# Kernel optimization log

Measured on AMD Instinct MI355X. Metric: run time of the kernel, lower is better.

## Reference

```python
import jax, jax.numpy as jnp
import numpy as np

N = 100000
E = 1600000
IN_DIM, HID, OUT = 128, 64, 32
SLOPE = 0.1


def setup_inputs() -> dict:
    key = jax.random.key(0)
    ks = jax.random.split(key, 8)
    x = jax.random.normal(ks[0], (N, IN_DIM), dtype=jnp.float32)
    edge_index = jax.random.randint(ks[1], (2, E), 0, N, dtype=jnp.int64)
    s1 = 1.0 / np.sqrt(IN_DIM)
    s2 = 1.0 / np.sqrt(HID)
    W_l1 = jax.random.uniform(ks[2], (IN_DIM, HID), jnp.float32, -s1, s1)
    W_r1 = jax.random.uniform(ks[3], (IN_DIM, HID), jnp.float32, -s1, s1)
    b1 = jax.random.uniform(ks[4], (HID,), jnp.float32, -s1, s1)
    W_l2 = jax.random.uniform(ks[5], (HID, OUT), jnp.float32, -s2, s2)
    W_r2 = jax.random.uniform(ks[6], (HID, OUT), jnp.float32, -s2, s2)
    b2 = jax.random.uniform(ks[7], (OUT,), jnp.float32, -s2, s2)
    return {"x": x, "edge_index": edge_index,
            "W_l1": W_l1, "W_r1": W_r1, "b1": b1,
            "W_l2": W_l2, "W_r2": W_r2, "b2": b2}


def _sage_conv(h, src, dst, deg_inv, W_l, W_r, b):
    # mean-aggregate neighbor features: gather from src, scatter-add to dst
    agg = jax.ops.segment_sum(h[src], dst, num_segments=N) * deg_inv  # [N, d]
    return agg @ W_l + h @ W_r + b


def reference(x, edge_index, W_l1, W_r1, b1, W_l2, W_r2, b2):
    src, dst = edge_index[0], edge_index[1]
    deg = jax.ops.segment_sum(jnp.ones((E,), x.dtype), dst, num_segments=N)
    deg_inv = (1.0 / jnp.maximum(deg, 1.0))[:, None]  # [N, 1]
    h = jax.nn.leaky_relu(_sage_conv(x, src, dst, deg_inv, W_l1, W_r1, b1), SLOPE)
    z = jax.nn.leaky_relu(_sage_conv(h, src, dst, deg_inv, W_l2, W_r2, b2), SLOPE)
    return z
```

## Files before the change

### kernel.cpp

```cpp
#include <hip/hip_runtime.h>


constexpr int IN_DIM  = 128;
constexpr int HID     = 64;
constexpr int OUT_DIM = 32;
constexpr float SLOPE = 0.1f;
constexpr int NPB_SHIFT = 8;
constexpr int NBMAX = 512;
constexpr int CHUNK = 4096;
constexpr int SUBCAP = 4096;

typedef unsigned int uint32;
typedef unsigned short ushort16;
typedef unsigned char uchar8;
using floatx2 = __attribute__((ext_vector_type(2))) float;

__device__ inline float blo(uint32 u) { return __uint_as_float(u << 16); }
__device__ inline float bhi(uint32 u) { return __uint_as_float(u & 0xffff0000u); }
__device__ inline ushort16 f2b(float f) {
    uint32 u = __float_as_uint(f);
    u += 0x7fffu + ((u >> 16) & 1u);
    return (ushort16)(u >> 16);
}
__device__ inline uint32 pack2(float lo, float hi) {
    return (uint32)f2b(lo) | ((uint32)f2b(hi) << 16);
}
__device__ inline float lrelu(float v) { return (v > 0.f) ? v : SLOPE * v; }
__device__ inline void addup(float* acc, uint4 u) {
    acc[0] += blo(u.x); acc[1] += bhi(u.x);
    acc[2] += blo(u.y); acc[3] += bhi(u.y);
    acc[4] += blo(u.z); acc[5] += bhi(u.z);
    acc[6] += blo(u.w); acc[7] += bhi(u.w);
}
__device__ inline uchar8 f2fp8(float f) {
    uint32 r = (uint32)__builtin_amdgcn_cvt_pk_fp8_f32(f, f, 0, false);
    return (uchar8)(r & 0xffu);
}
__device__ inline void addp4(float* acc, uint32 w) {
    floatx2 a = __builtin_amdgcn_cvt_pk_f32_fp8((int)w, false);
    floatx2 b = __builtin_amdgcn_cvt_pk_f32_fp8((int)w, true);
    acc[0] += a[0]; acc[1] += a[1]; acc[2] += b[0]; acc[3] += b[1];
}
__device__ inline void addq8(float* acc, uint2 u) {
    addp4(acc + 0, u.x); addp4(acc + 4, u.y);
}

__global__ __launch_bounds__(256) void prep_kernel(
    const float* __restrict__ Wl1, const float* __restrict__ Wr1,
    const float* __restrict__ Wl2, const float* __restrict__ Wr2,
    ushort16* __restrict__ Wb1, ushort16* __restrict__ Wb2,
    int* __restrict__ bhist, int* __restrict__ done) {
    const int gid = blockIdx.x * 256 + threadIdx.x;
    if (gid < NBMAX) bhist[gid] = 0;
    if (gid == NBMAX) *done = 0;
    for (int i = gid; i < 128 * 128; i += gridDim.x * 256) {
        int c = i >> 7, k = i & 127;
        Wb1[i] = f2b((c < HID) ? Wl1[k * HID + c] : Wr1[k * HID + (c - HID)]);
    }
    for (int i = gid; i < 64 * 64; i += gridDim.x * 256) {
        int c = i >> 6, k = i & 63;
        Wb2[i] = f2b((c < OUT_DIM) ? Wl2[k * OUT_DIM + c]
                                   : Wr2[k * OUT_DIM + (c - OUT_DIM)]);
    }
}

__global__ __launch_bounds__(256) void hist_scan_kernel(
    const int* __restrict__ dst, int* __restrict__ bhist,
    int* __restrict__ pbase, int* __restrict__ bcur,
    int* __restrict__ done, int E, int NB) {
    __shared__ int bh[NBMAX];
    __shared__ int s2[256];
    __shared__ int flag;
    const int tid = threadIdx.x;
    for (int i = tid; i < NBMAX; i += 256) bh[i] = 0;
    __syncthreads();
    for (int e = blockIdx.x * 256 + tid; e < E; e += gridDim.x * 256)
        atomicAdd(&bh[dst[e] >> NPB_SHIFT], 1);
    __syncthreads();
    for (int b = tid; b < NBMAX; b += 256)
        if (bh[b]) atomicAdd(&bhist[b], bh[b]);
    __threadfence();
    if (tid == 0) flag = (atomicAdd(done, 1) == (int)gridDim.x - 1) ? 1 : 0;
    __syncthreads();
    if (!flag) return;
    __threadfence();
    int v0 = atomicAdd(&bhist[2 * tid], 0);
    int v1 = atomicAdd(&bhist[2 * tid + 1], 0);
    int p0 = (v0 + 15) & ~15, p1 = (v1 + 15) & ~15;
    s2[tid] = p0 + p1; __syncthreads();
    for (int off = 1; off < 256; off <<= 1) {
        int b = (tid >= off) ? s2[tid - off] : 0;
        __syncthreads();
        s2[tid] += b;
        __syncthreads();
    }
    int base = s2[tid] - (p0 + p1);
    pbase[2 * tid]     = base;      bcur[2 * tid]     = base;
    pbase[2 * tid + 1] = base + p0; bcur[2 * tid + 1] = base + p0;
}

__global__ __launch_bounds__(256) void gemm1_part_kernel(
    const float* __restrict__ x, const ushort16* __restrict__ Wb1,
    const float* __restrict__ b1,
    const int* __restrict__ src, const int* __restrict__ dst,
    int* __restrict__ bcur, uint32* __restrict__ pairs,
    ushort16* __restrict__ xl, ushort16* __restrict__ xr,
    int N, int E, int NB, int npart) {
    using frag = __attribute__((ext_vector_type(8))) short;
    using f32x4 = __attribute__((ext_vector_type(4))) float;
    constexpr int LDA = IN_DIM + 8;
    __shared__ union {
        struct {
            int hist[NBMAX], loff[NBMAX], cur[NBMAX], gbase[NBMAX];
            int s[256];
            uint32 stage[CHUNK];
        } p;
        ushort16 Ash[64][LDA];
        ushort16 xst[2][64][64];
    } sm;
    const int tid = threadIdx.x;
    if (blockIdx.x < npart) {
        const int e0  = blockIdx.x * CHUNK;
        const int cnt = min(CHUNK, E - e0);
        for (int i = tid; i < NBMAX; i += 256) sm.p.hist[i] = 0;
        __syncthreads();
        int sreg[16], dreg[16];
#pragma unroll
        for (int k = 0; k < 16; ++k) {
            int i = tid + k * 256;
            if (i < cnt) {
                sreg[k] = src[e0 + i];
                dreg[k] = dst[e0 + i];
                atomicAdd(&sm.p.hist[dreg[k] >> NPB_SHIFT], 1);
            }
        }
        __syncthreads();
        int a0 = sm.p.hist[2 * tid], a1 = sm.p.hist[2 * tid + 1];
        sm.p.s[tid] = a0 + a1; __syncthreads();
        for (int off = 1; off < 256; off <<= 1) {
            int t = (tid >= off) ? sm.p.s[tid - off] : 0;
            __syncthreads();
            sm.p.s[tid] += t;
            __syncthreads();
        }
        int ex = sm.p.s[tid] - (a0 + a1);
        sm.p.loff[2 * tid] = ex;      sm.p.loff[2 * tid + 1] = ex + a0;
        sm.p.cur[2 * tid]  = ex;      sm.p.cur[2 * tid + 1]  = ex + a0;
        __syncthreads();
#pragma unroll
        for (int k = 0; k < 16; ++k) {
            int i = tid + k * 256;
            if (i < cnt) {
                int b = dreg[k] >> NPB_SHIFT;
                int pos = atomicAdd(&sm.p.cur[b], 1);
                sm.p.stage[pos] = (uint32)sreg[k] | ((uint32)(dreg[k] & 255) << 24);
            }
        }
        __syncthreads();
        for (int b = tid; b < NB; b += 256) {
            int cb = sm.p.hist[b];
            if (cb) sm.p.gbase[b] = atomicAdd(&bcur[b], cb);
        }
        __syncthreads();
        for (int i = tid; i < cnt; i += 256) {
            int lo = 0, hi = NB - 1;
            while (lo < hi) {
                int mid = (lo + hi + 1) >> 1;
                if (sm.p.loff[mid] <= i) lo = mid; else hi = mid - 1;
            }
            pairs[sm.p.gbase[lo] + (i - sm.p.loff[lo])] = sm.p.stage[i];
        }
        return;
    }
    const int n0 = (blockIdx.x - npart) * 64;
    {
        const int lc = (tid & 31) * 4;
        for (int row = tid >> 5; row < 64; row += 8) {
            int node = n0 + row;
            float4 xv = (node < N)
                ? *reinterpret_cast<const float4*>(&x[(long)node * IN_DIM + lc])
                : float4{0.f, 0.f, 0.f, 0.f};
            ushort16 pk[4] = {f2b(xv.x), f2b(xv.y), f2b(xv.z), f2b(xv.w)};
            *reinterpret_cast<ushort2*>(&sm.Ash[row][lc])     = ushort2{pk[0], pk[1]};
            *reinterpret_cast<ushort2*>(&sm.Ash[row][lc + 2]) = ushort2{pk[2], pk[3]};
        }
    }
    __syncthreads();
    const int lane = tid & 63;
    const int m0   = (tid >> 6) * 16;
    const int mlo  = lane & 15;
    const int qk   = lane >> 4;
    frag Af[4];
#pragma unroll
    for (int kc = 0; kc < 4; ++kc)
        Af[kc] = *reinterpret_cast<const frag*>(&sm.Ash[m0 + mlo][kc * 32 + qk * 8]);
    __syncthreads();
#pragma unroll
    for (int ct = 0; ct < 8; ++ct) {
        f32x4 acc = {0.f, 0.f, 0.f, 0.f};
#pragma unroll
        for (int kc = 0; kc < 4; ++kc) {
            frag Bf = *reinterpret_cast<const frag*>(
                &Wb1[(ct * 16 + mlo) * 128 + kc * 32 + qk * 8]);
            acc = __builtin_amdgcn_mfma_f32_16x16x32_bf16(Af[kc], Bf, acc, 0, 0, 0);
        }
        const int col = ct * 16 + mlo;
#pragma unroll
        for (int r = 0; r < 4; ++r) {
            int row = m0 + qk * 4 + r;
            if (col < HID) sm.xst[0][row][col] = f2b(acc[r]);
            else           sm.xst[1][row][col - HID] = f2b(acc[r] + b1[col - HID]);
        }
    }
    __syncthreads();
    for (int idx = tid; idx < 64 * 8; idx += 256) {
        int row = idx >> 3, ch = idx & 7;
        int node = n0 + row;
        if (node < N) {
            reinterpret_cast<uint4*>(xl)[(long)node * 8 + ch] =
                reinterpret_cast<const uint4*>(&sm.xst[0][0][0])[idx];
            reinterpret_cast<uint4*>(xr)[(long)node * 8 + ch] =
                reinterpret_cast<const uint4*>(&sm.xst[1][0][0])[idx];
        }
    }
}

__global__ __launch_bounds__(512) void agg1_gemm2_kernel(
    const uint32* __restrict__ pairs, const int* __restrict__ bhist,
    const int* __restrict__ pbase,
    const uint4* __restrict__ xlq, const uint4* __restrict__ xrq,
    const ushort16* __restrict__ Wb2, const float* __restrict__ b2,
    uint32* __restrict__ srcs, int* __restrict__ rowptr, int* __restrict__ degA,
    uchar8* __restrict__ hl8, ushort16* __restrict__ hr, int N) {
    using frag = __attribute__((ext_vector_type(8))) short;
    using f32x4 = __attribute__((ext_vector_type(4))) float;
    constexpr int LDH = HID + 8;
    __shared__ int hist[256], loff[256], cur[128];
    __shared__ int lsrc[SUBCAP];
    __shared__ ushort16 hsh[128][LDH];
    const int tid  = threadIdx.x;
    const int bkt  = blockIdx.x >> 1;
    const int half = blockIdx.x & 1;
    const int n0   = bkt << NPB_SHIFT;
    const int base = pbase[bkt];
    const int sz   = bhist[bkt];
    if (tid < 256) hist[tid] = 0;
    __syncthreads();
    for (int i = tid; i < sz; i += 512)
        atomicAdd(&hist[pairs[base + i] >> 24], 1);
    __syncthreads();
    int v = (tid < 256) ? hist[tid] : 0;
    if (tid < 256) loff[tid] = v;
    __syncthreads();
    for (int off = 1; off < 256; off <<= 1) {
        int t = (tid >= off && tid < 256) ? loff[tid - off] : 0;
        __syncthreads();
        if (tid < 256) loff[tid] += t;
        __syncthreads();
    }
    if (tid < 256) loff[tid] -= v;
    __syncthreads();
    if (half == 0 && tid < 256 && n0 + tid < N) {
        rowptr[n0 + tid] = base + loff[tid];
        degA[n0 + tid]   = hist[tid];
    }
    const int hbase = loff[half << 7];
    const int hcnt  = (half ? sz : loff[128]) - hbase;
    if (tid < 128) cur[tid] = loff[(half << 7) + tid] - hbase;
    __syncthreads();
    for (int i = tid; i < sz; i += 512) {
        uint32 u = pairs[base + i];
        int dl = u >> 24;
        if ((dl >> 7) == half) {
            int pos = atomicAdd(&cur[dl & 127], 1);
            lsrc[pos] = (int)(u & 0xFFFFFFu);
        }
    }
    __syncthreads();
    for (int i = tid; i < hcnt; i += 512)
        srcs[base + hbase + i] = (uint32)lsrc[i];
    const int lane = tid & 63;
    const int wid  = tid >> 6;
    const int li   = lane & 7;
#pragma unroll
    for (int pass = 0; pass < 2; ++pass) {
        const int nll = pass * 64 + wid * 8 + (lane >> 3);
        const int nl  = (half << 7) + nll;
        const int n   = n0 + nl;
        if (n >= N) continue;
        const int lo0 = loff[nl] - hbase;
        const int d   = hist[nl];
        float acc[8] = {};
        int j = 0;
        while (j + 16 <= d) {
            int i0[8], i1[8];
#pragma unroll
            for (int t = 0; t < 8; ++t) i0[t] = lsrc[lo0 + j + t];
#pragma unroll
            for (int t = 0; t < 8; ++t) i1[t] = lsrc[lo0 + j + 8 + t];
            uint4 u0[8], u1[8];
#pragma unroll
            for (int t = 0; t < 8; ++t) u0[t] = xlq[(long)i0[t] * 8 + li];
#pragma unroll
            for (int t = 0; t < 8; ++t) u1[t] = xlq[(long)i1[t] * 8 + li];
#pragma unroll
            for (int t = 0; t < 8; ++t) { addup(acc, u0[t]); addup(acc, u1[t]); }
            j += 16;
        }
        if (j + 8 <= d) {
            int i0[8];
#pragma unroll
            for (int t = 0; t < 8; ++t) i0[t] = lsrc[lo0 + j + t];
            uint4 u0[8];
#pragma unroll
            for (int t = 0; t < 8; ++t) u0[t] = xlq[(long)i0[t] * 8 + li];
#pragma unroll
            for (int t = 0; t < 8; ++t) addup(acc, u0[t]);
            j += 8;
        }
        for (; j < d; ++j) {
            uint4 u = xlq[(long)lsrc[lo0 + j] * 8 + li];
            addup(acc, u);
        }
        const float dinv = (d > 0) ? (1.f / (float)d) : 1.f;
        uint4 xv = xrq[(long)n * 8 + li];
        float h[8];
        h[0] = fmaf(acc[0], dinv, blo(xv.x)); h[1] = fmaf(acc[1], dinv, bhi(xv.x));
        h[2] = fmaf(acc[2], dinv, blo(xv.y)); h[3] = fmaf(acc[3], dinv, bhi(xv.y));
        h[4] = fmaf(acc[4], dinv, blo(xv.z)); h[5] = fmaf(acc[5], dinv, bhi(xv.z));
        h[6] = fmaf(acc[6], dinv, blo(xv.w)); h[7] = fmaf(acc[7], dinv, bhi(xv.w));
#pragma unroll
        for (int t = 0; t < 8; ++t) h[t] = lrelu(h[t]);
        uint4 pk;
        pk.x = pack2(h[0], h[1]); pk.y = pack2(h[2], h[3]);
        pk.z = pack2(h[4], h[5]); pk.w = pack2(h[6], h[7]);
        *reinterpret_cast<uint4*>(&hsh[nll][li * 8]) = pk;
    }
    __syncthreads();
    unsigned char* hl_st = reinterpret_cast<unsigned char*>(lsrc);
    ushort16* hr_st = reinterpret_cast<ushort16*>(lsrc + 1024);
    const int m0  = wid * 16;
    const int mlo = lane & 15;
    const int qk  = lane >> 4;
    frag Af[2];
#pragma unroll
    for (int kc = 0; kc < 2; ++kc)
        Af[kc] = *reinterpret_cast<const frag*>(&hsh[m0 + mlo][kc * 32 + qk * 8]);
#pragma unroll
    for (int ct = 0; ct < 4; ++ct) {
        f32x4 acc = {0.f, 0.f, 0.f, 0.f};
#pragma unroll
        for (int kc = 0; kc < 2; ++kc) {
            frag Bf = *reinterpret_cast<const frag*>(
                &Wb2[(ct * 16 + mlo) * 64 + kc * 32 + qk * 8]);
            acc = __builtin_amdgcn_mfma_f32_16x16x32_bf16(Af[kc], Bf, acc, 0, 0, 0);
        }
        const int col = ct * 16 + mlo;
#pragma unroll
        for (int r = 0; r < 4; ++r) {
            int row = m0 + qk * 4 + r;
            if (col < OUT_DIM) hl_st[row * 32 + col] = f2fp8(acc[r]);
            else hr_st[row * 32 + (col - OUT_DIM)] = f2b(acc[r] + b2[col - OUT_DIM]);
        }
    }
    __syncthreads();
    for (int idx = tid; idx < 128 * 2; idx += 512) {
        int row = idx >> 1, ch = idx & 1;
        int node = n0 + (half << 7) + row;
        if (node < N)
            reinterpret_cast<uint4*>(hl8)[(long)node * 2 + ch] =
                reinterpret_cast<const uint4*>(hl_st)[idx];
    }
    for (int idx = tid; idx < 128 * 4; idx += 512) {
        int row = idx >> 2, ch = idx & 3;
        int node = n0 + (half << 7) + row;
        if (node < N)
            reinterpret_cast<uint4*>(hr)[(long)node * 4 + ch] =
                reinterpret_cast<const uint4*>(hr_st)[idx];
    }
}

__global__ __launch_bounds__(256) void agg2_final_kernel(
    const int* __restrict__ rowptr, const int* __restrict__ degA,
    const uint32* __restrict__ srcs,
    const uint2* __restrict__ hlq, const uint4* __restrict__ hrq,
    float* __restrict__ z, int N) {
    const int lane  = threadIdx.x & 63;
    const int li    = lane & 3;
    const int gbase = lane & 60;
    const int wave  = (blockIdx.x << 2) + (threadIdx.x >> 6);
    const int n     = wave * 16 + (lane >> 2);
    if (n >= N) return;
    const int rp = rowptr[n];
    const int d  = degA[n];
    float acc[8] = {};
    int j = 0;
    while (j + 16 <= d) {
        int sA = (int)srcs[rp + j + li];
        int sB = (int)srcs[rp + j + 4 + li];
        int sC = (int)srcs[rp + j + 8 + li];
        int sD = (int)srcs[rp + j + 12 + li];
        uint2 u[16];
#pragma unroll
        for (int t = 0; t < 4; ++t) u[t]      = hlq[(long)__shfl(sA, gbase + t) * 4 + li];
#pragma unroll
        for (int t = 0; t < 4; ++t) u[4 + t]  = hlq[(long)__shfl(sB, gbase + t) * 4 + li];
#pragma unroll
        for (int t = 0; t < 4; ++t) u[8 + t]  = hlq[(long)__shfl(sC, gbase + t) * 4 + li];
#pragma unroll
        for (int t = 0; t < 4; ++t) u[12 + t] = hlq[(long)__shfl(sD, gbase + t) * 4 + li];
#pragma unroll
        for (int t = 0; t < 16; ++t) addq8(acc, u[t]);
        j += 16;
    }
    while (j + 4 <= d) {
        int sA = (int)srcs[rp + j + li];
        uint2 u[4];
#pragma unroll
        for (int t = 0; t < 4; ++t) u[t] = hlq[(long)__shfl(sA, gbase + t) * 4 + li];
#pragma unroll
        for (int t = 0; t < 4; ++t) addq8(acc, u[t]);
        j += 4;
    }
    int r = d - j;
    if (r > 0) {
        int sA = (int)srcs[rp + j + ((li < r) ? li : 0)];
#pragma unroll
        for (int t = 0; t < 3; ++t) {
            if (t < r) {
                uint2 u = hlq[(long)__shfl(sA, gbase + t) * 4 + li];
                addq8(acc, u);
            }
        }
    }
    const float dinv = (d > 0) ? (1.f / (float)d) : 1.f;
    uint4 hv = hrq[(long)n * 4 + li];
    float4 vA, vB;
    vA.x = lrelu(fmaf(acc[0], dinv, blo(hv.x))); vA.y = lrelu(fmaf(acc[1], dinv, bhi(hv.x)));
    vA.z = lrelu(fmaf(acc[2], dinv, blo(hv.y))); vA.w = lrelu(fmaf(acc[3], dinv, bhi(hv.y)));
    vB.x = lrelu(fmaf(acc[4], dinv, blo(hv.z))); vB.y = lrelu(fmaf(acc[5], dinv, bhi(hv.z)));
    vB.z = lrelu(fmaf(acc[6], dinv, blo(hv.w))); vB.w = lrelu(fmaf(acc[7], dinv, bhi(hv.w)));
    *reinterpret_cast<float4*>(&z[(long)n * OUT_DIM + 8 * li]) = vA;
    *reinterpret_cast<float4*>(&z[(long)n * OUT_DIM + 8 * li + 4]) = vB;
}

extern "C" void kernel_launch(void* const* d_in, const int* in_sizes, int n_in,
                              void* d_out, int out_size, void* d_ws, size_t ws_size,
                              hipStream_t stream) {
    const float* x   = (const float*)d_in[0];
    const int*   ei  = (const int*)d_in[1];
    const float* Wl1 = (const float*)d_in[2];
    const float* Wr1 = (const float*)d_in[3];
    const float* b1  = (const float*)d_in[4];
    const float* Wl2 = (const float*)d_in[5];
    const float* Wr2 = (const float*)d_in[6];
    const float* b2  = (const float*)d_in[7];

    const int N = in_sizes[0] / IN_DIM;
    const int E = in_sizes[1] / 2;
    const int* src = ei;
    const int* dst = ei + E;
    const int NB = (N + 255) >> NPB_SHIFT;

    char* p = (char*)d_ws;
    int* bhist    = (int*)p;           p += sizeof(int) * NBMAX;
    int* done     = (int*)p;           p += sizeof(int) * 4;
    int* pbase    = (int*)p;           p += sizeof(int) * NBMAX;
    int* bcur     = (int*)p;           p += sizeof(int) * NBMAX;
    int* rowptr   = (int*)p;           p += sizeof(int) * (N + 4);
    int* degA     = (int*)p;           p += sizeof(int) * (N + 4);
    uint32* pairs = (uint32*)p;        p += sizeof(uint32) * ((size_t)E + 16 * NBMAX);
    uint32* srcs  = (uint32*)p;        p += sizeof(uint32) * ((size_t)E + 16 * NBMAX);
    ushort16* Wb1 = (ushort16*)p;      p += sizeof(ushort16) * 128 * 128;
    ushort16* Wb2 = (ushort16*)p;      p += sizeof(ushort16) * 64 * 64;
    ushort16* xl  = (ushort16*)p;      p += sizeof(ushort16) * (size_t)N * HID;
    ushort16* xr  = (ushort16*)p;      p += sizeof(ushort16) * ((size_t)N * HID + 8);
    uchar8* hl8   = (uchar8*)p;        p += sizeof(uchar8) * ((size_t)N * OUT_DIM + 64);
    ushort16* hr  = (ushort16*)p;      p += sizeof(ushort16) * ((size_t)N * OUT_DIM + 8);

    const int ngemm = (N + 63) / 64;
    const int npart = (E + CHUNK - 1) / CHUNK;
    prep_kernel<<<32, 256, 0, stream>>>(Wl1, Wr1, Wl2, Wr2, Wb1, Wb2, bhist, done);
    hist_scan_kernel<<<256, 256, 0, stream>>>(dst, bhist, pbase, bcur, done, E, NB);
    gemm1_part_kernel<<<npart + ngemm, 256, 0, stream>>>(
        x, Wb1, b1, src, dst, bcur, pairs, xl, xr, N, E, NB, npart);
    agg1_gemm2_kernel<<<NB * 2, 512, 0, stream>>>(pairs, bhist, pbase,
                                                  (const uint4*)xl, (const uint4*)xr,
                                                  Wb2, b2,
                                                  srcs, rowptr, degA, hl8, hr, N);
    agg2_final_kernel<<<(N + 63) / 64, 256, 0, stream>>>(rowptr, degA, srcs,
                                                         (const uint2*)hl8,
                                                         (const uint4*)hr,
                                                         (float*)d_out, N);
}
```

Before: 259.8 us.

## Store layer-1 gather features in FP8 and build CSR rowptr via global degree scan

The neighbour-side layer-1 projection (xl) is now written as FP8 instead of bf16, which halves the bytes moved by the dominant edge-gather loop in the first aggregation. Degree counting also changes: a per-node global histogram, a two-kernel scan and a rowptr array are computed up front. This replaces the per-bucket histogram and scan that agg1 used to do, and drops the 16-element bucket padding. In exchange it uses 1.6M global atomics and two extra launches, and FP8 adds quantisation error to the layer-1 aggregate.

```diff
diff --git a/kernel.cpp b/kernel.cpp
--- a/kernel.cpp
+++ b/kernel.cpp
@@ -26,12 +26,6 @@
     return (uint32)f2b(lo) | ((uint32)f2b(hi) << 16);
 }
 __device__ inline float lrelu(float v) { return (v > 0.f) ? v : SLOPE * v; }
-__device__ inline void addup(float* acc, uint4 u) {
-    acc[0] += blo(u.x); acc[1] += bhi(u.x);
-    acc[2] += blo(u.y); acc[3] += bhi(u.y);
-    acc[4] += blo(u.z); acc[5] += bhi(u.z);
-    acc[6] += blo(u.w); acc[7] += bhi(u.w);
-}
 __device__ inline uchar8 f2fp8(float f) {
     uint32 r = (uint32)__builtin_amdgcn_cvt_pk_fp8_f32(f, f, 0, false);
     return (uchar8)(r & 0xffu);
@@ -49,54 +43,75 @@
     const float* __restrict__ Wl1, const float* __restrict__ Wr1,
     const float* __restrict__ Wl2, const float* __restrict__ Wr2,
     ushort16* __restrict__ Wb1, ushort16* __restrict__ Wb2,
-    int* __restrict__ bhist, int* __restrict__ done) {
+    int* __restrict__ deg, int* __restrict__ done2, int N) {
     const int gid = blockIdx.x * 256 + threadIdx.x;
-    if (gid < NBMAX) bhist[gid] = 0;
-    if (gid == NBMAX) *done = 0;
-    for (int i = gid; i < 128 * 128; i += gridDim.x * 256) {
+    const int stride = gridDim.x * 256;
+    for (int i = gid; i < N + 2; i += stride) deg[i] = 0;
+    if (gid == 0) *done2 = 0;
+    for (int i = gid; i < 128 * 128; i += stride) {
         int c = i >> 7, k = i & 127;
         Wb1[i] = f2b((c < HID) ? Wl1[k * HID + c] : Wr1[k * HID + (c - HID)]);
     }
-    for (int i = gid; i < 64 * 64; i += gridDim.x * 256) {
+    for (int i = gid; i < 64 * 64; i += stride) {
         int c = i >> 6, k = i & 63;
         Wb2[i] = f2b((c < OUT_DIM) ? Wl2[k * OUT_DIM + c]
                                    : Wr2[k * OUT_DIM + (c - OUT_DIM)]);
     }
 }
 
-__global__ __launch_bounds__(256) void hist_scan_kernel(
-    const int* __restrict__ dst, int* __restrict__ bhist,
-    int* __restrict__ pbase, int* __restrict__ bcur,
-    int* __restrict__ done, int E, int NB) {
-    __shared__ int bh[NBMAX];
-    __shared__ int s2[256];
+__global__ __launch_bounds__(256) void hist_kernel(
+    const int* __restrict__ dst, int* __restrict__ deg, int E) {
+    for (int e = blockIdx.x * 256 + threadIdx.x; e < E; e += gridDim.x * 256)
+        atomicAdd(&deg[dst[e]], 1);
+}
+
+__global__ __launch_bounds__(256) void scanA_kernel(
+    const int* __restrict__ deg, int* __restrict__ loc,
+    int* __restrict__ bsum, int* __restrict__ gbase,
+    int* __restrict__ done2, int N, int NBK) {
+    __shared__ int s[256];
     __shared__ int flag;
     const int tid = threadIdx.x;
-    for (int i = tid; i < NBMAX; i += 256) bh[i] = 0;
-    __syncthreads();
-    for (int e = blockIdx.x * 256 + tid; e < E; e += gridDim.x * 256)
-        atomicAdd(&bh[dst[e] >> NPB_SHIFT], 1);
-    __syncthreads();
-    for (int b = tid; b < NBMAX; b += 256)
-        if (bh[b]) atomicAdd(&bhist[b], bh[b]);
+    const int n = blockIdx.x * 256 + tid;
+    int v = (n < N) ? deg[n] : 0;
+    s[tid] = v; __syncthreads();
+    for (int off = 1; off < 256; off <<= 1) {
+        int t = (tid >= off) ? s[tid - off] : 0;
+        __syncthreads();
+        s[tid] += t;
+        __syncthreads();
+    }
+    if (n < N) loc[n] = s[tid] - v;
+    if (tid == 255) bsum[blockIdx.x] = s[255];
     __threadfence();
-    if (tid == 0) flag = (atomicAdd(done, 1) == (int)gridDim.x - 1) ? 1 : 0;
+    if (tid == 0) flag = (atomicAdd(done2, 1) == NBK - 1) ? 1 : 0;
     __syncthreads();
     if (!flag) return;
     __threadfence();
-    int v0 = atomicAdd(&bhist[2 * tid], 0);
-    int v1 = atomicAdd(&bhist[2 * tid + 1], 0);
-    int p0 = (v0 + 15) & ~15, p1 = (v1 + 15) & ~15;
-    s2[tid] = p0 + p1; __syncthreads();
+    int v0 = (2 * tid     < NBK) ? atomicAdd(&bsum[2 * tid], 0)     : 0;
+    int v1 = (2 * tid + 1 < NBK) ? atomicAdd(&bsum[2 * tid + 1], 0) : 0;
+    s[tid] = v0 + v1; __syncthreads();
     for (int off = 1; off < 256; off <<= 1) {
-        int b = (tid >= off) ? s2[tid - off] : 0;
-        __syncthreads();
-        s2[tid] += b;
-        __syncthreads();
-    }
-    int base = s2[tid] - (p0 + p1);
-    pbase[2 * tid]     = base;      bcur[2 * tid]     = base;
-    pbase[2 * tid + 1] = base + p0; bcur[2 * tid + 1] = base + p0;
+        int t = (tid >= off) ? s[tid - off] : 0;
+        __syncthreads();
+        s[tid] += t;
+        __syncthreads();
+    }
+    int base = s[tid] - (v0 + v1);
+    if (2 * tid     < NBK) gbase[2 * tid]     = base;
+    if (2 * tid + 1 < NBK) gbase[2 * tid + 1] = base + v0;
+}
+
+__global__ __launch_bounds__(256) void scanB_kernel(
+    const int* __restrict__ loc, const int* __restrict__ gbase,
+    int* __restrict__ rowptr, int* __restrict__ bcur, int N, int E) {
+    const int n = blockIdx.x * 256 + threadIdx.x;
+    if (n < N) {
+        int r = gbase[n >> 8] + loc[n];
+        rowptr[n] = r;
+        if ((n & 255) == 0) bcur[n >> 8] = r;
+    }
+    if (n == 0) rowptr[N] = E;
 }
 
 __global__ __launch_bounds__(256) void gemm1_part_kernel(
@@ -104,7 +119,7 @@
     const float* __restrict__ b1,
     const int* __restrict__ src, const int* __restrict__ dst,
     int* __restrict__ bcur, uint32* __restrict__ pairs,
-    ushort16* __restrict__ xl, ushort16* __restrict__ xr,
+    uchar8* __restrict__ xl8, ushort16* __restrict__ xr,
     int N, int E, int NB, int npart) {
     using frag = __attribute__((ext_vector_type(8))) short;
     using f32x4 = __attribute__((ext_vector_type(4))) float;
@@ -116,7 +131,7 @@
             uint32 stage[CHUNK];
         } p;
         ushort16 Ash[64][LDA];
-        ushort16 xst[2][64][64];
+        struct { uchar8 xl[64][64]; ushort16 xr[64][64]; } o;
     } sm;
     const int tid = threadIdx.x;
     if (blockIdx.x < npart) {
@@ -208,65 +223,56 @@
 #pragma unroll
         for (int r = 0; r < 4; ++r) {
             int row = m0 + qk * 4 + r;
-            if (col < HID) sm.xst[0][row][col] = f2b(acc[r]);
-            else           sm.xst[1][row][col - HID] = f2b(acc[r] + b1[col - HID]);
-        }
-    }
-    __syncthreads();
+            if (col < HID) sm.o.xl[row][col] = f2fp8(acc[r]);
+            else           sm.o.xr[row][col - HID] = f2b(acc[r] + b1[col - HID]);
+        }
+    }
+    __syncthreads();
+    for (int idx = tid; idx < 64 * 4; idx += 256) {
+        int row = idx >> 2, ch = idx & 3;
+        int node = n0 + row;
+        if (node < N)
+            reinterpret_cast<uint4*>(xl8)[(long)node * 4 + ch] =
+                reinterpret_cast<const uint4*>(&sm.o.xl[0][0])[idx];
+    }
     for (int idx = tid; idx < 64 * 8; idx += 256) {
         int row = idx >> 3, ch = idx & 7;
         int node = n0 + row;
-        if (node < N) {
-            reinterpret_cast<uint4*>(xl)[(long)node * 8 + ch] =
-                reinterpret_cast<const uint4*>(&sm.xst[0][0][0])[idx];
+        if (node < N)
             reinterpret_cast<uint4*>(xr)[(long)node * 8 + ch] =
-                reinterpret_cast<const uint4*>(&sm.xst[1][0][0])[idx];
-        }
+                reinterpret_cast<const uint4*>(&sm.o.xr[0][0])[idx];
     }
 }
 
 __global__ __launch_bounds__(512) void agg1_gemm2_kernel(
-    const uint32* __restrict__ pairs, const int* __restrict__ bhist,
-    const int* __restrict__ pbase,
-    const uint4* __restrict__ xlq, const uint4* __restrict__ xrq,
+    const uint32* __restrict__ pairs, const int* __restrict__ rowptr,
+    const uint2* __restrict__ xlq, const uint4* __restrict__ xrq,
     const ushort16* __restrict__ Wb2, const float* __restrict__ b2,
-    uint32* __restrict__ srcs, int* __restrict__ rowptr, int* __restrict__ degA,
-    uchar8* __restrict__ hl8, ushort16* __restrict__ hr, int N) {
+    uint32* __restrict__ srcs, uchar8* __restrict__ hl8,
+    ushort16* __restrict__ hr, int N) {
     using frag = __attribute__((ext_vector_type(8))) short;
     using f32x4 = __attribute__((ext_vector_type(4))) float;
     constexpr int LDH = HID + 8;
-    __shared__ int hist[256], loff[256], cur[128];
+    __shared__ int rps[129], cur[128];
     __shared__ int lsrc[SUBCAP];
     __shared__ ushort16 hsh[128][LDH];
     const int tid  = threadIdx.x;
     const int bkt  = blockIdx.x >> 1;
     const int half = blockIdx.x & 1;
     const int n0   = bkt << NPB_SHIFT;
-    const int base = pbase[bkt];
-    const int sz   = bhist[bkt];
-    if (tid < 256) hist[tid] = 0;
-    __syncthreads();
-    for (int i = tid; i < sz; i += 512)
-        atomicAdd(&hist[pairs[base + i] >> 24], 1);
-    __syncthreads();
-    int v = (tid < 256) ? hist[tid] : 0;
-    if (tid < 256) loff[tid] = v;
-    __syncthreads();
-    for (int off = 1; off < 256; off <<= 1) {
-        int t = (tid >= off && tid < 256) ? loff[tid - off] : 0;
-        __syncthreads();
-        if (tid < 256) loff[tid] += t;
-        __syncthreads();
-    }
-    if (tid < 256) loff[tid] -= v;
-    __syncthreads();
-    if (half == 0 && tid < 256 && n0 + tid < N) {
-        rowptr[n0 + tid] = base + loff[tid];
-        degA[n0 + tid]   = hist[tid];
-    }
-    const int hbase = loff[half << 7];
-    const int hcnt  = (half ? sz : loff[128]) - hbase;
-    if (tid < 128) cur[tid] = loff[(half << 7) + tid] - hbase;
+    const int hstart = n0 + (half << 7);
+    if (tid < 129) {
+        int nn = hstart + tid;
+        rps[tid] = rowptr[nn < N ? nn : N];
+    }
+    __syncthreads();
+    const int base = rowptr[min(n0 + 256, N) - min(256, 0)] * 0 +
+                     rowptr[n0 < N ? n0 : N];
+    const int bend = rowptr[min(n0 + 256, N)];
+    const int sz   = bend - base;
+    const int hb   = rps[0];
+    const int hcnt = rps[128] - hb;
+    if (tid < 128) cur[tid] = rps[tid] - hb;
     __syncthreads();
     for (int i = tid; i < sz; i += 512) {
         uint32 u = pairs[base + i];
@@ -278,18 +284,17 @@
     }
     __syncthreads();
     for (int i = tid; i < hcnt; i += 512)
-        srcs[base + hbase + i] = (uint32)lsrc[i];
+        srcs[hb + i] = (uint32)lsrc[i];
     const int lane = tid & 63;
     const int wid  = tid >> 6;
     const int li   = lane & 7;
 #pragma unroll
     for (int pass = 0; pass < 2; ++pass) {
         const int nll = pass * 64 + wid * 8 + (lane >> 3);
-        const int nl  = (half << 7) + nll;
-        const int n   = n0 + nl;
+        const int n   = hstart + nll;
         if (n >= N) continue;
-        const int lo0 = loff[nl] - hbase;
-        const int d   = hist[nl];
+        const int lo0 = rps[nll] - hb;
+        const int d   = rps[nll + 1] - rps[nll];
         float acc[8] = {};
         int j = 0;
         while (j + 16 <= d) {
@@ -298,29 +303,29 @@
             for (int t = 0; t < 8; ++t) i0[t] = lsrc[lo0 + j + t];
 #pragma unroll
             for (int t = 0; t < 8; ++t) i1[t] = lsrc[lo0 + j + 8 + t];
-            uint4 u0[8], u1[8];
+            uint2 u0[8], u1[8];
 #pragma unroll
             for (int t = 0; t < 8; ++t) u0[t] = xlq[(long)i0[t] * 8 + li];
 #pragma unroll
             for (int t = 0; t < 8; ++t) u1[t] = xlq[(long)i1[t] * 8 + li];
 #pragma unroll
-            for (int t = 0; t < 8; ++t) { addup(acc, u0[t]); addup(acc, u1[t]); }
+            for (int t = 0; t < 8; ++t) { addq8(acc, u0[t]); addq8(acc, u1[t]); }
             j += 16;
         }
         if (j + 8 <= d) {
             int i0[8];
 #pragma unroll
             for (int t = 0; t < 8; ++t) i0[t] = lsrc[lo0 + j + t];
-            uint4 u0[8];
+            uint2 u0[8];
 #pragma unroll
             for (int t = 0; t < 8; ++t) u0[t] = xlq[(long)i0[t] * 8 + li];
 #pragma unroll
-            for (int t = 0; t < 8; ++t) addup(acc, u0[t]);
+            for (int t = 0; t < 8; ++t) addq8(acc, u0[t]);
             j += 8;
         }
         for (; j < d; ++j) {
-            uint4 u = xlq[(long)lsrc[lo0 + j] * 8 + li];
-            addup(acc, u);
+            uint2 u = xlq[(long)lsrc[lo0 + j] * 8 + li];
+            addq8(acc, u);
         }
         const float dinv = (d > 0) ? (1.f / (float)d) : 1.f;
         uint4 xv = xrq[(long)n * 8 + li];
@@ -366,14 +371,14 @@
     __syncthreads();
     for (int idx = tid; idx < 128 * 2; idx += 512) {
         int row = idx >> 1, ch = idx & 1;
-        int node = n0 + (half << 7) + row;
+        int node = hstart + row;
         if (node < N)
             reinterpret_cast<uint4*>(hl8)[(long)node * 2 + ch] =
                 reinterpret_cast<const uint4*>(hl_st)[idx];
     }
     for (int idx = tid; idx < 128 * 4; idx += 512) {
         int row = idx >> 2, ch = idx & 3;
-        int node = n0 + (half << 7) + row;
+        int node = hstart + row;
         if (node < N)
             reinterpret_cast<uint4*>(hr)[(long)node * 4 + ch] =
                 reinterpret_cast<const uint4*>(hr_st)[idx];
@@ -381,7 +386,7 @@
 }
 
 __global__ __launch_bounds__(256) void agg2_final_kernel(
-    const int* __restrict__ rowptr, const int* __restrict__ degA,
+    const int* __restrict__ rowptr, const int* __restrict__ deg,
     const uint32* __restrict__ srcs,
     const uint2* __restrict__ hlq, const uint4* __restrict__ hrq,
     float* __restrict__ z, int N) {
@@ -392,7 +397,7 @@
     const int n     = wave * 16 + (lane >> 2);
     if (n >= N) return;
     const int rp = rowptr[n];
-    const int d  = degA[n];
+    const int d  = deg[n];
     float acc[8] = {};
     int j = 0;
     while (j + 16 <= d) {
@@ -460,35 +465,38 @@
     const int E = in_sizes[1] / 2;
     const int* src = ei;
     const int* dst = ei + E;
-    const int NB = (N + 255) >> NPB_SHIFT;
+    const int NB  = (N + 255) >> NPB_SHIFT;
+    const int NBK = NB;
 
     char* p = (char*)d_ws;
-    int* bhist    = (int*)p;           p += sizeof(int) * NBMAX;
-    int* done     = (int*)p;           p += sizeof(int) * 4;
-    int* pbase    = (int*)p;           p += sizeof(int) * NBMAX;
+    int* deg      = (int*)p;           p += sizeof(int) * (N + 4);
+    int* loc      = (int*)p;           p += sizeof(int) * (N + 4);
+    int* rowptr   = (int*)p;           p += sizeof(int) * (N + 4);
+    int* bsum     = (int*)p;           p += sizeof(int) * NBMAX;
+    int* gbase    = (int*)p;           p += sizeof(int) * NBMAX;
     int* bcur     = (int*)p;           p += sizeof(int) * NBMAX;
-    int* rowptr   = (int*)p;           p += sizeof(int) * (N + 4);
-    int* degA     = (int*)p;           p += sizeof(int) * (N + 4);
-    uint32* pairs = (uint32*)p;        p += sizeof(uint32) * ((size_t)E + 16 * NBMAX);
-    uint32* srcs  = (uint32*)p;        p += sizeof(uint32) * ((size_t)E + 16 * NBMAX);
+    int* done2    = (int*)p;           p += sizeof(int) * 4;
+    uint32* pairs = (uint32*)p;        p += sizeof(uint32) * ((size_t)E + 16);
+    uint32* srcs  = (uint32*)p;        p += sizeof(uint32) * ((size_t)E + 16);
     ushort16* Wb1 = (ushort16*)p;      p += sizeof(ushort16) * 128 * 128;
     ushort16* Wb2 = (ushort16*)p;      p += sizeof(ushort16) * 64 * 64;
-    ushort16* xl  = (ushort16*)p;      p += sizeof(ushort16) * (size_t)N * HID;
+    uchar8* xl8   = (uchar8*)p;        p += sizeof(uchar8) * ((size_t)N * HID + 64);
     ushort16* xr  = (ushort16*)p;      p += sizeof(ushort16) * ((size_t)N * HID + 8);
     uchar8* hl8   = (uchar8*)p;        p += sizeof(uchar8) * ((size_t)N * OUT_DIM + 64);
     ushort16* hr  = (ushort16*)p;      p += sizeof(ushort16) * ((size_t)N * OUT_DIM + 8);
 
     const int ngemm = (N + 63) / 64;
     const int npart = (E + CHUNK - 1) / CHUNK;
-    prep_kernel<<<32, 256, 0, stream>>>(Wl1, Wr1, Wl2, Wr2, Wb1, Wb2, bhist, done);
-    hist_scan_kernel<<<256, 256, 0, stream>>>(dst, bhist, pbase, bcur, done, E, NB);
+    prep_kernel<<<96, 256, 0, stream>>>(Wl1, Wr1, Wl2, Wr2, Wb1, Wb2, deg, done2, N);
+    hist_kernel<<<512, 256, 0, stream>>>(dst, deg, E);
+    scanA_kernel<<<NBK, 256, 0, stream>>>(deg, loc, bsum, gbase, done2, N, NBK);
+    scanB_kernel<<<NBK, 256, 0, stream>>>(loc, gbase, rowptr, bcur, N, E);
     gemm1_part_kernel<<<npart + ngemm, 256, 0, stream>>>(
-        x, Wb1, b1, src, dst, bcur, pairs, xl, xr, N, E, NB, npart);
-    agg1_gemm2_kernel<<<NB * 2, 512, 0, stream>>>(pairs, bhist, pbase,
-                                                  (const uint4*)xl, (const uint4*)xr,
-                                                  Wb2, b2,
-                                                  srcs, rowptr, degA, hl8, hr, N);
-    agg2_final_kernel<<<(N + 63) / 64, 256, 0, stream>>>(rowptr, degA, srcs,
+        x, Wb1, b1, src, dst, bcur, pairs, xl8, xr, N, E, NB, npart);
+    agg1_gemm2_kernel<<<NB * 2, 512, 0, stream>>>(pairs, rowptr,
+                                                  (const uint2*)xl8, (const uint4*)xr,
+                                                  Wb2, b2, srcs, hl8, hr, N);
+    agg2_final_kernel<<<(N + 63) / 64, 256, 0, stream>>>(rowptr, deg, srcs,
                                                          (const uint2*)hl8,
                                                          (const uint4*)hr,
                                                          (float*)d_out, N);
```

Result: slower. 310.4 us (+19.5%).
